# Kernel tuning notes

Measured on AMD Instinct MI355X. Metric: run time of the kernel, lower is better.

## Reference

```python
import jax, jax.numpy as jnp
import numpy as np

N = 100000      # nodes
E = 1600000     # edges (no self-loops by construction)
DIN, DH, DOUT = 128, 128, 64
EPS = 1e-8      # torch cosine_similarity eps
LN_EPS = 1e-5


def _segsum(v, idx, n=N):
    return jax.ops.segment_sum(v, idx, num_segments=n)


def att_coef(feats, row, col):
    """Edge-wise cosine-sim attention + degree norm + self-loop append (torch no_grad block).
    Returns fixed-shape (row2, col2, vals2) of length E+N; filtered edges get weight 0
    (equivalent to removal for all scatter_add / message-passing math)."""
    dot = jnp.einsum('ed,ed->e', feats[row], feats[col])            # [E]
    nrm = jnp.maximum(jnp.linalg.norm(feats, axis=1), EPS)          # [N]
    sims = dot / (nrm[row] * nrm[col])
    keep = sims >= 0.1                                              # row!=col guaranteed
    sims = jnp.where(keep, sims, 0.0)
    deg = _segsum(sims, row)
    dinv = jnp.where(deg > 0, deg ** -0.5, 0.0)                     # inf -> 0
    sims = dinv[row] * sims * dinv[col]
    deg_new = _segsum(keep.astype(feats.dtype), col) + 1.0          # [N], >= 1
    self_val = 1.0 / deg_new
    vals = jnp.where(keep, jnp.exp(sims), 0.0)                      # removed edges -> 0
    sl = jnp.arange(N)
    row2 = jnp.concatenate([row, sl])
    col2 = jnp.concatenate([col, sl])
    vals2 = jnp.concatenate([vals, jnp.exp(self_val)])
    return row2, col2, vals2


def gcn_conv(x, row, col, w, W, b):
    """PyG GCNConv (normalize=True, add_self_loops=False) with given edge_weight."""
    h = x @ W                                                        # [N, out]
    deg = _segsum(w, col)
    dinv = jnp.where(deg > 0, deg ** -0.5, 0.0)
    norm = dinv[row] * w * dinv[col]                                 # [E+N]
    out = _segsum(norm[:, None] * h[row], col)                       # scatter to targets
    return out + b


def layer_norm(x, g, b):
    mu = jnp.mean(x, axis=-1, keepdims=True)
    var = jnp.mean((x - mu) ** 2, axis=-1, keepdims=True)
    return (x - mu) * jax.lax.rsqrt(var + LN_EPS) * g + b


def setup_inputs() -> dict:
    key = jax.random.key(0)
    ks = jax.random.split(key, 6)
    x = jax.random.normal(ks[0], (N, DIN), jnp.float32)
    row = jax.random.randint(ks[1], (E,), 0, N)
    col = jax.random.randint(ks[2], (E,), 0, N)
    col = jnp.where(col == row, (col + 1) % N, col)                  # no self-loops
    s1 = float(np.sqrt(6.0 / (DIN + DH)))                            # glorot
    s2 = float(np.sqrt(6.0 / (DH + DOUT)))
    W1 = jax.random.uniform(ks[3], (DIN, DH), jnp.float32, -s1, s1)
    W2 = jax.random.uniform(ks[4], (DH, DOUT), jnp.float32, -s2, s2)
    return dict(x=x, row=row, col=col,
                W1=W1, b1=jnp.zeros((DH,), jnp.float32),
                ln_g=jnp.ones((DH,), jnp.float32), ln_b=jnp.zeros((DH,), jnp.float32),
                W2=W2, b2=jnp.zeros((DOUT,), jnp.float32))


def reference(x, row, col, W1, b1, ln_g, ln_b, W2, b2):
    # layer 1: att_coef (no_grad) -> GCNConv -> LayerNorm -> ReLU (dropout is eval no-op)
    r2, c2, v2 = att_coef(jax.lax.stop_gradient(x), row, col)
    h = gcn_conv(x, r2, c2, v2, W1, b1)
    h = jax.nn.relu(layer_norm(h, ln_g, ln_b))
    # layer 2: att_coef on updated features (original edge list), final conv + log_softmax
    r2, c2, v2 = att_coef(jax.lax.stop_gradient(h), row, col)
    out = gcn_conv(h, r2, c2, v2, W2, b2)
    return jax.nn.log_softmax(out, axis=-1)
```

## Files before the change

### kernel.cpp

```cpp
#include <hip/hip_runtime.h>
#include <math.h>

#define EPSF 1e-8f
#define LN_EPS 1e-5f
#define BL_MARGIN 0.002f

typedef unsigned int  u32;
typedef unsigned short u16;
typedef _Float16 h2_t __attribute__((ext_vector_type(2)));
typedef _Float16 half8_t __attribute__((ext_vector_type(8)));
typedef float f32x4_t __attribute__((ext_vector_type(4)));

static __device__ inline u32 pack_h2(float a, float b) {
    h2_t h; h.x = (_Float16)a; h.y = (_Float16)b;
    return __builtin_bit_cast(u32, h);
}
static __device__ inline float h2lo(u32 u) {
    return (float)__builtin_bit_cast(h2_t, u).x;
}
static __device__ inline float h2hi(u32 u) {
    return (float)__builtin_bit_cast(h2_t, u).y;
}

static __device__ inline f32x4_t mfma16(uint4 a, uint4 b, f32x4_t c) {
    return __builtin_amdgcn_mfma_f32_16x16x32_f16(
        __builtin_bit_cast(half8_t, a), __builtin_bit_cast(half8_t, b), c, 0, 0, 0);
}

__global__ __launch_bounds__(256) void cast_norm_k(const float* __restrict__ feat,
    u32* __restrict__ fhf, float* __restrict__ nrm, int n) {
    int wid  = (blockIdx.x * 256 + threadIdx.x) >> 6;
    int lane = threadIdx.x & 63;
    if (wid >= n) return;
    float2 v = *(const float2*)(feat + (size_t)wid * 128 + lane * 2);
    float s = v.x * v.x + v.y * v.y;
    #pragma unroll
    for (int off = 32; off; off >>= 1) s += __shfl_xor(s, off, 64);
    float nv = fmaxf(sqrtf(s), EPSF);
    float inv = 1.0f / nv;
    fhf[(size_t)wid * 64 + lane] = pack_h2(v.x * inv, v.y * inv);
    if (lane == 0) nrm[wid] = nv;
}


__global__ __launch_bounds__(256) void count_k(const int* __restrict__ col,
                                               int* __restrict__ cntAll, int ecnt) {
    int e = blockIdx.x * 256 + threadIdx.x;
    if (e < ecnt) atomicAdd(&cntAll[col[e]], 1);
}

__global__ __launch_bounds__(256) void scan1_k(const int* __restrict__ cnt,
    int* __restrict__ colStart, int* __restrict__ bsum, int n) {
    __shared__ int tmp[256];
    int i = blockIdx.x * 256 + threadIdx.x;
    int v = (i < n) ? cnt[i] : 0;
    tmp[threadIdx.x] = v; __syncthreads();
    for (int off = 1; off < 256; off <<= 1) {
        int t = (threadIdx.x >= off) ? tmp[threadIdx.x - off] : 0;
        __syncthreads();
        tmp[threadIdx.x] += t;
        __syncthreads();
    }
    if (i < n) colStart[i] = tmp[threadIdx.x] - v;
    if (threadIdx.x == 255) bsum[blockIdx.x] = tmp[255];
}

__global__ __launch_bounds__(512) void scan2_k(int* __restrict__ bsum, int nb) {
    __shared__ int tmp[512];
    int v = (threadIdx.x < nb) ? bsum[threadIdx.x] : 0;
    tmp[threadIdx.x] = v; __syncthreads();
    for (int off = 1; off < 512; off <<= 1) {
        int t = (threadIdx.x >= off) ? tmp[threadIdx.x - off] : 0;
        __syncthreads();
        tmp[threadIdx.x] += t;
        __syncthreads();
    }
    if (threadIdx.x < nb) bsum[threadIdx.x] = tmp[threadIdx.x] - v;
}

__global__ __launch_bounds__(256) void scan3_k(int* __restrict__ colStart,
    const int* __restrict__ bsum, int n) {
    int i = blockIdx.x * 256 + threadIdx.x;
    if (i < n) colStart[i] += bsum[blockIdx.x];
}

__global__ __launch_bounds__(256) void fill_k(const int* __restrict__ row,
    const int* __restrict__ col, const int* __restrict__ startAll,
    int* __restrict__ cur, int* __restrict__ rowAll, int ecnt) {
    int e = blockIdx.x * 256 + threadIdx.x;
    if (e >= ecnt) return;
    int c = col[e];
    int p = startAll[c] + atomicAdd(&cur[c], 1);
    rowAll[p] = row[e];
}

__global__ __launch_bounds__(256) void edge_dot_mf_k(const u32* __restrict__ fhf,
    const float* __restrict__ feat32,
    const int* __restrict__ rowAll, const int* __restrict__ startAll,
    const int* __restrict__ cntAll, const float* __restrict__ nrm,
    float* __restrict__ sims, float* __restrict__ deg1, int n) {
    int wid  = (blockIdx.x * 256 + threadIdx.x) >> 6;
    int lane = threadIdx.x & 63;
    if (wid >= n) return;
    int s0 = startAll[wid], cnt = cntAll[wid];
    if (cnt == 0) return;
    int lr = lane & 15;
    int kq = lane >> 4;
    const u32* fcp = fhf + (size_t)wid * 64 + kq * 4;
    uint4 a0 = *(const uint4*)(fcp);
    uint4 a1 = *(const uint4*)(fcp + 16);
    uint4 a2 = *(const uint4*)(fcp + 32);
    uint4 a3 = *(const uint4*)(fcp + 48);
    float nc = nrm[wid];
    int cm1 = cnt - 1;
    for (int jj = 0; jj < cnt; jj += 32) {
        int e1 = jj + lr;
        int r1 = rowAll[s0 + min(e1, cm1)];
        const u32* fr1 = fhf + (size_t)r1 * 64 + kq * 4;
        uint4 b0 = *(const uint4*)(fr1);
        uint4 b1 = *(const uint4*)(fr1 + 16);
        uint4 b2 = *(const uint4*)(fr1 + 32);
        uint4 b3 = *(const uint4*)(fr1 + 48);
        bool g2 = (jj + 16) < cnt;
        int e2 = jj + 16 + lr;
        int r2 = 0;
        uint4 c0, c1, c2, c3;
        if (g2) {
            r2 = rowAll[s0 + min(e2, cm1)];
            const u32* fr2 = fhf + (size_t)r2 * 64 + kq * 4;
            c0 = *(const uint4*)(fr2);
            c1 = *(const uint4*)(fr2 + 16);
            c2 = *(const uint4*)(fr2 + 32);
            c3 = *(const uint4*)(fr2 + 48);
        }
        f32x4_t acc = {0.f, 0.f, 0.f, 0.f};
        acc = mfma16(a0, b0, acc);
        acc = mfma16(a1, b1, acc);
        acc = mfma16(a2, b2, acc);
        acc = mfma16(a3, b3, acc);
        float p1 = acc[0];
        bool act1 = (kq == 0) && (e1 < cnt);
        float p2 = 0.0f;
        bool act2 = false;
        if (g2) {
            f32x4_t acc2 = {0.f, 0.f, 0.f, 0.f};
            acc2 = mfma16(a0, c0, acc2);
            acc2 = mfma16(a1, c1, acc2);
            acc2 = mfma16(a2, c2, acc2);
            acc2 = mfma16(a3, c3, acc2);
            p2 = acc2[0];
            act2 = (kq == 0) && (e2 < cnt);
        }
        unsigned long long bl = __ballot(act1 && fabsf(p1 - 0.1f) < BL_MARGIN);
        while (bl) {
            int src = __ffsll((unsigned long long)bl) - 1; bl &= bl - 1ull;
            int rt = __shfl(r1, src, 64);
            float2 xa = *(const float2*)(feat32 + (size_t)rt * 128 + lane * 2);
            float2 xb = *(const float2*)(feat32 + (size_t)wid * 128 + lane * 2);
            float s2 = xa.x * xb.x + xa.y * xb.y;
            #pragma unroll
            for (int off = 32; off; off >>= 1) s2 += __shfl_xor(s2, off, 64);
            float pf = s2 / (nrm[rt] * nc);
            if (lane == src) p1 = pf;
        }
        unsigned long long bl2 = __ballot(act2 && fabsf(p2 - 0.1f) < BL_MARGIN);
        while (bl2) {
            int src = __ffsll((unsigned long long)bl2) - 1; bl2 &= bl2 - 1ull;
            int rt = __shfl(r2, src, 64);
            float2 xa = *(const float2*)(feat32 + (size_t)rt * 128 + lane * 2);
            float2 xb = *(const float2*)(feat32 + (size_t)wid * 128 + lane * 2);
            float s2 = xa.x * xb.x + xa.y * xb.y;
            #pragma unroll
            for (int off = 32; off; off >>= 1) s2 += __shfl_xor(s2, off, 64);
            float pf = s2 / (nrm[rt] * nc);
            if (lane == src) p2 = pf;
        }
        if (act1) {
            float kv = (p1 >= 0.1f) ? p1 : 0.0f;
            sims[s0 + e1] = kv;
            if (kv > 0.0f) atomicAdd(&deg1[r1], kv);
        }
        if (act2) {
            float kv = (p2 >= 0.1f) ? p2 : 0.0f;
            sims[s0 + e2] = kv;
            if (kv > 0.0f) atomicAdd(&deg1[r2], kv);
        }
    }
}

__global__ __launch_bounds__(256) void edge_c_csr_k(const float* __restrict__ sims,
    const int* __restrict__ rowAll, const int* __restrict__ startAll,
    const int* __restrict__ cntAll, const float* __restrict__ deg1,
    int2* __restrict__ kv, int* __restrict__ cntK, float* __restrict__ dinv2,
    float* __restrict__ cself, int n) {
    int wid  = (blockIdx.x * 256 + threadIdx.x) >> 6;
    int lane = threadIdx.x & 63;
    if (wid >= n) return;
    int s0 = startAll[wid], cnt = cntAll[wid];
    float degc = deg1[wid];
    float d1c = (degc > 0.0f) ? 1.0f / sqrtf(degc) : 0.0f;
    float vsum = 0.0f; int kc = 0;
    for (int jj = 0; jj < cnt; jj += 64) {
        int j = jj + lane;
        bool keep = false; int r = 0; float v = 0.0f;
        if (j < cnt) {
            float s = sims[s0 + j];
            if (s > 0.0f) {
                r = rowAll[s0 + j];
                float dr = 1.0f / sqrtf(deg1[r]);
                v = expf(dr * s * d1c);
                keep = true;
            }
        }
        unsigned long long m = __ballot(keep ? 1 : 0);
        if (keep) {
            int pre = __popcll(m & ((1ull << lane) - 1ull));
            int2 pk; pk.x = r; pk.y = __float_as_int(v);
            kv[s0 + kc + pre] = pk;
            vsum += v;
        }
        kc += __popcll(m);
    }
    #pragma unroll
    for (int off = 32; off; off >>= 1) vsum += __shfl_xor(vsum, off, 64);
    if (lane == 0) {
        float ws_ = expf(1.0f / ((float)kc + 1.0f));
        float dg = ws_ + vsum;
        float di = 1.0f / sqrtf(dg);
        dinv2[wid] = di;
        cself[wid] = di * ws_;
        cntK[wid]  = kc;
    }
}


__global__ __launch_bounds__(256) void gemm128_k(const float* __restrict__ A,
    const float* __restrict__ W, const float* __restrict__ scale,
    float* __restrict__ out, int n) {
    __shared__ float Ws[128 * 64];
    int colBase = blockIdx.y * 64;
    for (int i = threadIdx.x; i < 128 * 64 / 4; i += 256) {
        int k = i >> 4, c4 = i & 15;
        ((float4*)Ws)[i] = *(const float4*)(W + k * 128 + colBase + c4 * 4);
    }
    __syncthreads();
    const int TPN = 16;
    int group = threadIdx.x / TPN;
    int tin   = threadIdx.x % TPN;
    int nid   = (blockIdx.x * 16 + group) * 4;
    if (nid >= n) return;
    int dbase = tin * 4;
    int nm1 = n - 1;
    const float4* a0 = (const float4*)(A + (size_t)min(nid,     nm1) * 128);
    const float4* a1 = (const float4*)(A + (size_t)min(nid + 1, nm1) * 128);
    const float4* a2 = (const float4*)(A + (size_t)min(nid + 2, nm1) * 128);
    const float4* a3 = (const float4*)(A + (size_t)min(nid + 3, nm1) * 128);
    float4 acc0 = {0,0,0,0}, acc1 = {0,0,0,0}, acc2 = {0,0,0,0}, acc3 = {0,0,0,0};
    #pragma unroll 2
    for (int k4 = 0; k4 < 32; ++k4) {
        const float* wr = Ws + (k4 * 4) * 64 + dbase;
        float4 w0 = *(const float4*)(wr);
        float4 w1 = *(const float4*)(wr + 64);
        float4 w2 = *(const float4*)(wr + 128);
        float4 w3 = *(const float4*)(wr + 192);
        float4 v0 = a0[k4], v1 = a1[k4], v2 = a2[k4], v3 = a3[k4];
        acc0.x += v0.x*w0.x + v0.y*w1.x + v0.z*w2.x + v0.w*w3.x;
        acc0.y += v0.x*w0.y + v0.y*w1.y + v0.z*w2.y + v0.w*w3.y;
        acc0.z += v0.x*w0.z + v0.y*w1.z + v0.z*w2.z + v0.w*w3.z;
        acc0.w += v0.x*w0.w + v0.y*w1.w + v0.z*w2.w + v0.w*w3.w;
        acc1.x += v1.x*w0.x + v1.y*w1.x + v1.z*w2.x + v1.w*w3.x;
        acc1.y += v1.x*w0.y + v1.y*w1.y + v1.z*w2.y + v1.w*w3.y;
        acc1.z += v1.x*w0.z + v1.y*w1.z + v1.z*w2.z + v1.w*w3.z;
        acc1.w += v1.x*w0.w + v1.y*w1.w + v1.z*w2.w + v1.w*w3.w;
        acc2.x += v2.x*w0.x + v2.y*w1.x + v2.z*w2.x + v2.w*w3.x;
        acc2.y += v2.x*w0.y + v2.y*w1.y + v2.z*w2.y + v2.w*w3.y;
        acc2.z += v2.x*w0.z + v2.y*w1.z + v2.z*w2.z + v2.w*w3.z;
        acc2.w += v2.x*w0.w + v2.y*w1.w + v2.z*w2.w + v2.w*w3.w;
        acc3.x += v3.x*w0.x + v3.y*w1.x + v3.z*w2.x + v3.w*w3.x;
        acc3.y += v3.x*w0.y + v3.y*w1.y + v3.z*w2.y + v3.w*w3.y;
        acc3.z += v3.x*w0.z + v3.y*w1.z + v3.z*w2.z + v3.w*w3.z;
        acc3.w += v3.x*w0.w + v3.y*w1.w + v3.z*w2.w + v3.w*w3.w;
    }
    float4 accs[4] = {acc0, acc1, acc2, acc3};
    #pragma unroll
    for (int i = 0; i < 4; ++i) {
        if (nid + i < n) {
            float sc = scale[nid + i];
            float4 r; r.x = accs[i].x * sc; r.y = accs[i].y * sc;
            r.z = accs[i].z * sc; r.w = accs[i].w * sc;
            *(float4*)(out + (size_t)(nid + i) * 128 + colBase + dbase) = r;
        }
    }
}

__global__ __launch_bounds__(256) void gemm64_hf_k(const float* __restrict__ A,
    const float* __restrict__ W, const float* __restrict__ scale,
    u32* __restrict__ outhf, int n) {
    __shared__ float Ws[128 * 32];
    int colBase = blockIdx.y * 32;
    for (int i = threadIdx.x; i < 128 * 32 / 4; i += 256) {
        int k = i >> 3, c4 = i & 7;
        ((float4*)Ws)[i] = *(const float4*)(W + k * 64 + colBase + c4 * 4);
    }
    __syncthreads();
    const int TPN = 8;
    int group = threadIdx.x / TPN;
    int tin   = threadIdx.x % TPN;
    int nid   = (blockIdx.x * 32 + group) * 4;
    if (nid >= n) return;
    int dbase = tin * 4;
    int nm1 = n - 1;
    const float4* a0 = (const float4*)(A + (size_t)min(nid,     nm1) * 128);
    const float4* a1 = (const float4*)(A + (size_t)min(nid + 1, nm1) * 128);
    const float4* a2 = (const float4*)(A + (size_t)min(nid + 2, nm1) * 128);
    const float4* a3 = (const float4*)(A + (size_t)min(nid + 3, nm1) * 128);
    float4 acc0 = {0,0,0,0}, acc1 = {0,0,0,0}, acc2 = {0,0,0,0}, acc3 = {0,0,0,0};
    #pragma unroll 2
    for (int k4 = 0; k4 < 32; ++k4) {
        const float* wr = Ws + (k4 * 4) * 32 + dbase;
        float4 w0 = *(const float4*)(wr);
        float4 w1 = *(const float4*)(wr + 32);
        float4 w2 = *(const float4*)(wr + 64);
        float4 w3 = *(const float4*)(wr + 96);
        float4 v0 = a0[k4], v1 = a1[k4], v2 = a2[k4], v3 = a3[k4];
        acc0.x += v0.x*w0.x + v0.y*w1.x + v0.z*w2.x + v0.w*w3.x;
        acc0.y += v0.x*w0.y + v0.y*w1.y + v0.z*w2.y + v0.w*w3.y;
        acc0.z += v0.x*w0.z + v0.y*w1.z + v0.z*w2.z + v0.w*w3.z;
        acc0.w += v0.x*w0.w + v0.y*w1.w + v0.z*w2.w + v0.w*w3.w;
        acc1.x += v1.x*w0.x + v1.y*w1.x + v1.z*w2.x + v1.w*w3.x;
        acc1.y += v1.x*w0.y + v1.y*w1.y + v1.z*w2.y + v1.w*w3.y;
        acc1.z += v1.x*w0.z + v1.y*w1.z + v1.z*w2.z + v1.w*w3.z;
        acc1.w += v1.x*w0.w + v1.y*w1.w + v1.z*w2.w + v1.w*w3.w;
        acc2.x += v2.x*w0.x + v2.y*w1.x + v2.z*w2.x + v2.w*w3.x;
        acc2.y += v2.x*w0.y + v2.y*w1.y + v2.z*w2.y + v2.w*w3.y;
        acc2.z += v2.x*w0.z + v2.y*w1.z + v2.z*w2.z + v2.w*w3.z;
        acc2.w += v2.x*w0.w + v2.y*w1.w + v2.z*w2.w + v2.w*w3.w;
        acc3.x += v3.x*w0.x + v3.y*w1.x + v3.z*w2.x + v3.w*w3.x;
        acc3.y += v3.x*w0.y + v3.y*w1.y + v3.z*w2.y + v3.w*w3.y;
        acc3.z += v3.x*w0.z + v3.y*w1.z + v3.z*w2.z + v3.w*w3.z;
        acc3.w += v3.x*w0.w + v3.y*w1.w + v3.z*w2.w + v3.w*w3.w;
    }
    float4 accs[4] = {acc0, acc1, acc2, acc3};
    #pragma unroll
    for (int i = 0; i < 4; ++i) {
        if (nid + i < n) {
            float sc = scale[nid + i];
            u32 o0 = pack_h2(accs[i].x * sc, accs[i].y * sc);
            u32 o1 = pack_h2(accs[i].z * sc, accs[i].w * sc);
            *(uint2*)(outhf + (size_t)(nid + i) * 32 + (colBase >> 1) + tin * 2)
                = make_uint2(o0, o1);
        }
    }
}


__global__ __launch_bounds__(256) void gather_ln_k(const float* __restrict__ hs,
    const int2* __restrict__ kv, const int* __restrict__ startAll,
    const int* __restrict__ cntK, const float* __restrict__ dinv2,
    const float* __restrict__ cself, const float* __restrict__ bias,
    const float* __restrict__ g, const float* __restrict__ bln,
    float* __restrict__ outbuf, u32* __restrict__ outhf,
    float* __restrict__ nrm, int n) {
    int wid = (blockIdx.x * 256 + threadIdx.x) >> 5;
    int l   = threadIdx.x & 31;
    if (wid >= n) return;
    int s0 = startAll[wid], k = cntK[wid];
    float4 acc = {0,0,0,0};
    int j = 0;
    for (; j + 7 < k; j += 8) {
        int2 p0 = kv[s0+j],   p1 = kv[s0+j+1], p2 = kv[s0+j+2], p3 = kv[s0+j+3];
        int2 p4 = kv[s0+j+4], p5 = kv[s0+j+5], p6 = kv[s0+j+6], p7 = kv[s0+j+7];
        float4 h0 = *(const float4*)(hs + (size_t)p0.x * 128 + l * 4);
        float4 h1 = *(const float4*)(hs + (size_t)p1.x * 128 + l * 4);
        float4 h2v = *(const float4*)(hs + (size_t)p2.x * 128 + l * 4);
        float4 h3 = *(const float4*)(hs + (size_t)p3.x * 128 + l * 4);
        float4 h4 = *(const float4*)(hs + (size_t)p4.x * 128 + l * 4);
        float4 h5 = *(const float4*)(hs + (size_t)p5.x * 128 + l * 4);
        float4 h6 = *(const float4*)(hs + (size_t)p6.x * 128 + l * 4);
        float4 h7 = *(const float4*)(hs + (size_t)p7.x * 128 + l * 4);
        float v0 = __int_as_float(p0.y), v1 = __int_as_float(p1.y);
        float v2 = __int_as_float(p2.y), v3 = __int_as_float(p3.y);
        float v4 = __int_as_float(p4.y), v5 = __int_as_float(p5.y);
        float v6 = __int_as_float(p6.y), v7 = __int_as_float(p7.y);
        acc.x += v0*h0.x + v1*h1.x + v2*h2v.x + v3*h3.x
               + v4*h4.x + v5*h5.x + v6*h6.x + v7*h7.x;
        acc.y += v0*h0.y + v1*h1.y + v2*h2v.y + v3*h3.y
               + v4*h4.y + v5*h5.y + v6*h6.y + v7*h7.y;
        acc.z += v0*h0.z + v1*h1.z + v2*h2v.z + v3*h3.z
               + v4*h4.z + v5*h5.z + v6*h6.z + v7*h7.z;
        acc.w += v0*h0.w + v1*h1.w + v2*h2v.w + v3*h3.w
               + v4*h4.w + v5*h5.w + v6*h6.w + v7*h7.w;
    }
    for (; j < k; ++j) {
        int2 p0 = kv[s0 + j];
        float4 h0 = *(const float4*)(hs + (size_t)p0.x * 128 + l * 4);
        float v0 = __int_as_float(p0.y);
        acc.x += v0*h0.x; acc.y += v0*h0.y; acc.z += v0*h0.z; acc.w += v0*h0.w;
    }
    float di = dinv2[wid], cs = cself[wid];
    float4 hsv = *(const float4*)(hs + (size_t)wid * 128 + l * 4);
    float4 vb  = *(const float4*)(bias + l * 4);
    float x0 = di*acc.x + cs*hsv.x + vb.x;
    float x1 = di*acc.y + cs*hsv.y + vb.y;
    float x2 = di*acc.z + cs*hsv.z + vb.z;
    float x3 = di*acc.w + cs*hsv.w + vb.w;
    float s = x0 + x1 + x2 + x3;
    #pragma unroll
    for (int off = 16; off; off >>= 1) s += __shfl_xor(s, off, 64);
    float mu = s * (1.0f / 128.0f);
    float d0 = x0 - mu, d1 = x1 - mu, d2 = x2 - mu, d3 = x3 - mu;
    float vv = d0*d0 + d1*d1 + d2*d2 + d3*d3;
    #pragma unroll
    for (int off = 16; off; off >>= 1) vv += __shfl_xor(vv, off, 64);
    float rstd = 1.0f / sqrtf(vv * (1.0f / 128.0f) + LN_EPS);
    float4 vg  = *(const float4*)(g + l * 4);
    float4 vbl = *(const float4*)(bln + l * 4);
    float y0 = fmaxf(d0 * rstd * vg.x + vbl.x, 0.0f);
    float y1 = fmaxf(d1 * rstd * vg.y + vbl.y, 0.0f);
    float y2 = fmaxf(d2 * rstd * vg.z + vbl.z, 0.0f);
    float y3 = fmaxf(d3 * rstd * vg.w + vbl.w, 0.0f);
    float4 yo; yo.x = y0; yo.y = y1; yo.z = y2; yo.w = y3;
    *(float4*)(outbuf + (size_t)wid * 128 + l * 4) = yo;
    float ns = y0*y0 + y1*y1 + y2*y2 + y3*y3;
    #pragma unroll
    for (int off = 16; off; off >>= 1) ns += __shfl_xor(ns, off, 64);
    float nv = fmaxf(sqrtf(ns), EPSF);
    float inv = 1.0f / nv;
    uint2 oh; oh.x = pack_h2(y0 * inv, y1 * inv); oh.y = pack_h2(y2 * inv, y3 * inv);
    *(uint2*)(outhf + (size_t)wid * 64 + l * 2) = oh;
    if (l == 0) nrm[wid] = nv;
}

__global__ __launch_bounds__(256) void gather_lsm_hf_k(const u32* __restrict__ g2s,
    const int2* __restrict__ kv, const int* __restrict__ startAll,
    const int* __restrict__ cntK, const float* __restrict__ dinv2,
    const float* __restrict__ cself, const float* __restrict__ b2,
    float* __restrict__ out, int n) {
    int wid = (blockIdx.x * 256 + threadIdx.x) >> 5;
    int l   = threadIdx.x & 31;
    if (wid >= n) return;
    int s0 = startAll[wid], k = cntK[wid];
    float acc0 = 0.f, acc1 = 0.f;
    int j = 0;
    for (; j + 7 < k; j += 8) {
        int2 p0 = kv[s0+j],   p1 = kv[s0+j+1], p2 = kv[s0+j+2], p3 = kv[s0+j+3];
        int2 p4 = kv[s0+j+4], p5 = kv[s0+j+5], p6 = kv[s0+j+6], p7 = kv[s0+j+7];
        u32 g0 = g2s[(size_t)p0.x * 32 + l];
        u32 g1 = g2s[(size_t)p1.x * 32 + l];
        u32 g2 = g2s[(size_t)p2.x * 32 + l];
        u32 g3 = g2s[(size_t)p3.x * 32 + l];
        u32 g4 = g2s[(size_t)p4.x * 32 + l];
        u32 g5 = g2s[(size_t)p5.x * 32 + l];
        u32 g6 = g2s[(size_t)p6.x * 32 + l];
        u32 g7 = g2s[(size_t)p7.x * 32 + l];
        float v0 = __int_as_float(p0.y), v1 = __int_as_float(p1.y);
        float v2 = __int_as_float(p2.y), v3 = __int_as_float(p3.y);
        float v4 = __int_as_float(p4.y), v5 = __int_as_float(p5.y);
        float v6 = __int_as_float(p6.y), v7 = __int_as_float(p7.y);
        acc0 += v0*h2lo(g0) + v1*h2lo(g1) + v2*h2lo(g2) + v3*h2lo(g3)
              + v4*h2lo(g4) + v5*h2lo(g5) + v6*h2lo(g6) + v7*h2lo(g7);
        acc1 += v0*h2hi(g0) + v1*h2hi(g1) + v2*h2hi(g2) + v3*h2hi(g3)
              + v4*h2hi(g4) + v5*h2hi(g5) + v6*h2hi(g6) + v7*h2hi(g7);
    }
    for (; j < k; ++j) {
        int2 p0 = kv[s0 + j];
        u32 g0 = g2s[(size_t)p0.x * 32 + l];
        float v0 = __int_as_float(p0.y);
        acc0 += v0 * h2lo(g0); acc1 += v0 * h2hi(g0);
    }
    float di = dinv2[wid], cs = cself[wid];
    u32 gsu = g2s[(size_t)wid * 32 + l];
    float2 vb = *(const float2*)(b2 + l * 2);
    float v0 = di * acc0 + cs * h2lo(gsu) + vb.x;
    float v1 = di * acc1 + cs * h2hi(gsu) + vb.y;
    float m = fmaxf(v0, v1);
    #pragma unroll
    for (int off = 16; off; off >>= 1) m = fmaxf(m, __shfl_xor(m, off, 64));
    float e = expf(v0 - m) + expf(v1 - m);
    #pragma unroll
    for (int off = 16; off; off >>= 1) e += __shfl_xor(e, off, 64);
    float lse = m + logf(e);
    *(float2*)(out + (size_t)wid * 64 + l * 2) = make_float2(v0 - lse, v1 - lse);
}


extern "C" void kernel_launch(void* const* d_in, const int* in_sizes, int n_in,
                              void* d_out, int out_size, void* d_ws, size_t ws_size,
                              hipStream_t stream) {
    (void)n_in; (void)out_size; (void)ws_size;
    const float* x   = (const float*)d_in[0];
    const int*   row = (const int*)d_in[1];
    const int*   col = (const int*)d_in[2];
    const float* W1  = (const float*)d_in[3];
    const float* b1  = (const float*)d_in[4];
    const float* lng = (const float*)d_in[5];
    const float* lnb = (const float*)d_in[6];
    const float* W2  = (const float*)d_in[7];
    const float* b2  = (const float*)d_in[8];
    float* out = (float*)d_out;

    const int N = in_sizes[0] / 128;
    const int E = in_sizes[1];

    int*   cntAll   = (int*)d_ws;
    int*   startAll = cntAll + N;
    int*   bsum     = startAll + N;
    float* nrm      = (float*)(bsum + 512);
    float* deg1     = nrm + N;
    float* dinv2    = deg1 + N;
    float* cself    = dinv2 + N;
    int*   cntK     = (int*)(cself + N);
    int*   rowAll   = cntK + N;
    int2*  kvp      = (int2*)(rowAll + E);
    u32*   fhf      = (u32*)(kvp + E);
    u32*   g2shf    = fhf + (size_t)64 * N;
    float* big      = (float*)(g2shf + (size_t)32 * N);
    float* sims     = big;
    float* hs       = big;
    float* h2       = big + (size_t)128 * N;

    const int nodeBlocks  = (N + 255) / 256;
    const int waveBlocks  = (N + 3) / 4;
    const int halfBlocks  = (N + 7) / 8;
    const int edgeBlocks  = (E + 255) / 256;
    const int scanBlocks  = nodeBlocks;

    hipMemsetAsync(cntAll, 0, (size_t)N * sizeof(int), stream);
    count_k<<<edgeBlocks, 256, 0, stream>>>(col, cntAll, E);
    scan1_k<<<scanBlocks, 256, 0, stream>>>(cntAll, startAll, bsum, N);
    scan2_k<<<1, 512, 0, stream>>>(bsum, scanBlocks);
    scan3_k<<<scanBlocks, 256, 0, stream>>>(startAll, bsum, N);
    hipMemsetAsync(cntK, 0, (size_t)N * sizeof(int), stream);
    fill_k<<<edgeBlocks, 256, 0, stream>>>(row, col, startAll, cntK, rowAll, E);

    hipMemsetAsync(deg1, 0, (size_t)N * sizeof(float), stream);
    cast_norm_k<<<waveBlocks, 256, 0, stream>>>(x, fhf, nrm, N);
    edge_dot_mf_k<<<waveBlocks, 256, 0, stream>>>(fhf, x, rowAll, startAll, cntAll, nrm,
                                                  sims, deg1, N);
    edge_c_csr_k<<<waveBlocks, 256, 0, stream>>>(sims, rowAll, startAll, cntAll, deg1,
                                                 kvp, cntK, dinv2, cself, N);
    gemm128_k<<<dim3((N + 63) / 64, 2), 256, 0, stream>>>(x, W1, dinv2, hs, N);
    gather_ln_k<<<halfBlocks, 256, 0, stream>>>(hs, kvp, startAll, cntK, dinv2, cself,
                                                b1, lng, lnb, h2, fhf, nrm, N);

    hipMemsetAsync(deg1, 0, (size_t)N * sizeof(float), stream);
    edge_dot_mf_k<<<waveBlocks, 256, 0, stream>>>(fhf, h2, rowAll, startAll, cntAll, nrm,
                                                  sims, deg1, N);
    edge_c_csr_k<<<waveBlocks, 256, 0, stream>>>(sims, rowAll, startAll, cntAll, deg1,
                                                 kvp, cntK, dinv2, cself, N);
    gemm64_hf_k<<<dim3((N + 127) / 128, 2), 256, 0, stream>>>(h2, W2, dinv2, g2shf, N);
    gather_lsm_hf_k<<<halfBlocks, 256, 0, stream>>>(g2shf, kvp, startAll, cntK, dinv2,
                                                    cself, b2, out, N);
}
```

Before: 720.0 us.

## Build CSR via two-level bucket sort instead of global atomic counting sort

```diff
diff --git a/kernel.cpp b/kernel.cpp
--- a/kernel.cpp
+++ b/kernel.cpp
@@ -4,6 +4,10 @@
 #define EPSF 1e-8f
 #define LN_EPS 1e-5f
 #define BL_MARGIN 0.002f
+
+#define BKT_SH 9
+#define CHUNK 4096
+#define DCAP 16384
 
 typedef unsigned int  u32;
 typedef unsigned short u16;
@@ -43,55 +47,136 @@
 }
 
 
-__global__ __launch_bounds__(256) void count_k(const int* __restrict__ col,
-                                               int* __restrict__ cntAll, int ecnt) {
-    int e = blockIdx.x * 256 + threadIdx.x;
-    if (e < ecnt) atomicAdd(&cntAll[col[e]], 1);
-}
-
-__global__ __launch_bounds__(256) void scan1_k(const int* __restrict__ cnt,
-    int* __restrict__ colStart, int* __restrict__ bsum, int n) {
+__global__ __launch_bounds__(256) void hist_k(const int* __restrict__ col,
+                                              int* __restrict__ bcnt, int ecnt) {
+    __shared__ int lc[256];
+    lc[threadIdx.x] = 0; __syncthreads();
+    for (int e = blockIdx.x * 256 + threadIdx.x; e < ecnt; e += gridDim.x * 256)
+        atomicAdd(&lc[col[e] >> BKT_SH], 1);
+    __syncthreads();
+    int v = lc[threadIdx.x];
+    if (v) atomicAdd(&bcnt[threadIdx.x], v);
+}
+
+__global__ __launch_bounds__(256) void bscan_k(const int* __restrict__ bcnt,
+    int* __restrict__ bstart, int* __restrict__ bcur) {
     __shared__ int tmp[256];
-    int i = blockIdx.x * 256 + threadIdx.x;
-    int v = (i < n) ? cnt[i] : 0;
-    tmp[threadIdx.x] = v; __syncthreads();
+    int t = threadIdx.x;
+    int v = bcnt[t];
+    tmp[t] = v; __syncthreads();
     for (int off = 1; off < 256; off <<= 1) {
-        int t = (threadIdx.x >= off) ? tmp[threadIdx.x - off] : 0;
+        int a = (t >= off) ? tmp[t - off] : 0;
         __syncthreads();
-        tmp[threadIdx.x] += t;
+        tmp[t] += a;
         __syncthreads();
     }
-    if (i < n) colStart[i] = tmp[threadIdx.x] - v;
-    if (threadIdx.x == 255) bsum[blockIdx.x] = tmp[255];
-}
-
-__global__ __launch_bounds__(512) void scan2_k(int* __restrict__ bsum, int nb) {
-    __shared__ int tmp[512];
-    int v = (threadIdx.x < nb) ? bsum[threadIdx.x] : 0;
-    tmp[threadIdx.x] = v; __syncthreads();
-    for (int off = 1; off < 512; off <<= 1) {
-        int t = (threadIdx.x >= off) ? tmp[threadIdx.x - off] : 0;
+    int ex = tmp[t] - v;
+    bstart[t] = ex; bcur[t] = ex;
+    if (t == 255) bstart[256] = tmp[255];
+}
+
+__global__ __launch_bounds__(256) void binfill_k(const int* __restrict__ row,
+    const int* __restrict__ col, int* __restrict__ bcur,
+    int2* __restrict__ ebuf, int ecnt) {
+    __shared__ int lc[256], ls[256], cur[256], gbase[256];
+    __shared__ int2 pairs[CHUNK];
+    __shared__ int dstv[CHUNK];
+    int t = threadIdx.x;
+    int e0 = blockIdx.x * CHUNK;
+    int m = min(CHUNK, ecnt - e0);
+    lc[t] = 0; cur[t] = 0; __syncthreads();
+    int myc[CHUNK / 256], myr[CHUNK / 256];
+    #pragma unroll
+    for (int i = 0; i < CHUNK / 256; ++i) {
+        int idx = t + i * 256;
+        if (idx < m) {
+            myc[i] = col[e0 + idx];
+            myr[i] = row[e0 + idx];
+            atomicAdd(&lc[myc[i] >> BKT_SH], 1);
+        }
+    }
+    __syncthreads();
+    int v = lc[t];
+    ls[t] = v; __syncthreads();
+    for (int off = 1; off < 256; off <<= 1) {
+        int a = (t >= off) ? ls[t - off] : 0;
         __syncthreads();
-        tmp[threadIdx.x] += t;
+        ls[t] += a;
         __syncthreads();
     }
-    if (threadIdx.x < nb) bsum[threadIdx.x] = tmp[threadIdx.x] - v;
-}
-
-__global__ __launch_bounds__(256) void scan3_k(int* __restrict__ colStart,
-    const int* __restrict__ bsum, int n) {
-    int i = blockIdx.x * 256 + threadIdx.x;
-    if (i < n) colStart[i] += bsum[blockIdx.x];
-}
-
-__global__ __launch_bounds__(256) void fill_k(const int* __restrict__ row,
-    const int* __restrict__ col, const int* __restrict__ startAll,
-    int* __restrict__ cur, int* __restrict__ rowAll, int ecnt) {
-    int e = blockIdx.x * 256 + threadIdx.x;
-    if (e >= ecnt) return;
-    int c = col[e];
-    int p = startAll[c] + atomicAdd(&cur[c], 1);
-    rowAll[p] = row[e];
+    int ex = ls[t] - v;
+    __syncthreads();
+    ls[t] = ex;
+    if (v) gbase[t] = atomicAdd(&bcur[t], v);
+    __syncthreads();
+    #pragma unroll
+    for (int i = 0; i < CHUNK / 256; ++i) {
+        int idx = t + i * 256;
+        if (idx < m) {
+            int b = myc[i] >> BKT_SH;
+            int s = ls[b] + atomicAdd(&cur[b], 1);
+            pairs[s] = make_int2(myc[i], myr[i]);
+            dstv[s]  = gbase[b] + (s - ls[b]);
+        }
+    }
+    __syncthreads();
+    for (int s = t; s < m; s += 256)
+        ebuf[dstv[s]] = pairs[s];
+}
+
+__global__ __launch_bounds__(256) void bucket_csr_k(const int2* __restrict__ ebuf,
+    const int* __restrict__ bstart, int* __restrict__ startAll,
+    int* __restrict__ cntAll, int* __restrict__ rowAll, int n) {
+    __shared__ int cnt[512], lst[512], cur[512];
+    __shared__ int rowbuf[DCAP];
+    int b = blockIdx.x, t = threadIdx.x;
+    int c0 = b << BKT_SH;
+    int s0 = bstart[b], s1 = bstart[b + 1];
+    int m = s1 - s0;
+    cnt[t] = 0; cnt[t + 256] = 0; cur[t] = 0; cur[t + 256] = 0;
+    __syncthreads();
+    for (int i = t; i < m; i += 256)
+        atomicAdd(&cnt[ebuf[s0 + i].x - c0], 1);
+    __syncthreads();
+    int v0 = cnt[t], v1 = cnt[t + 256];
+    lst[t] = v0; lst[t + 256] = v1; __syncthreads();
+    for (int off = 1; off < 256; off <<= 1) {
+        int a0 = (t >= off) ? lst[t - off] : 0;
+        int a1 = (t >= off) ? lst[256 + t - off] : 0;
+        __syncthreads();
+        lst[t] += a0; lst[t + 256] += a1;
+        __syncthreads();
+    }
+    int h0 = lst[255];
+    int e0x = lst[t] - v0;
+    int e1x = lst[t + 256] - v1 + h0;
+    __syncthreads();
+    lst[t] = e0x; lst[t + 256] = e1x;
+    __syncthreads();
+    #pragma unroll
+    for (int half = 0; half < 2; ++half) {
+        int i = t + half * 256;
+        int c = c0 + i;
+        if (c < n) { startAll[c] = s0 + lst[i]; cntAll[c] = cnt[i]; }
+    }
+    if (m <= DCAP) {
+        for (int i = t; i < m; i += 256) {
+            int2 p = ebuf[s0 + i];
+            int ci = p.x - c0;
+            int pos = lst[ci] + atomicAdd(&cur[ci], 1);
+            rowbuf[pos] = p.y;
+        }
+        __syncthreads();
+        for (int i = t; i < m; i += 256)
+            rowAll[s0 + i] = rowbuf[i];
+    } else {
+        for (int i = t; i < m; i += 256) {
+            int2 p = ebuf[s0 + i];
+            int ci = p.x - c0;
+            int pos = lst[ci] + atomicAdd(&cur[ci], 1);
+            rowAll[s0 + pos] = p.y;
+        }
+    }
 }
 
 __global__ __launch_bounds__(256) void edge_dot_mf_k(const u32* __restrict__ fhf,
@@ -504,8 +589,10 @@
 
     int*   cntAll   = (int*)d_ws;
     int*   startAll = cntAll + N;
-    int*   bsum     = startAll + N;
-    float* nrm      = (float*)(bsum + 512);
+    int*   bcnt     = startAll + N;
+    int*   bstart   = bcnt + 256;
+    int*   bcur     = bstart + 257;
+    float* nrm      = (float*)(bcnt + 1024);
     float* deg1     = nrm + N;
     float* dinv2    = deg1 + N;
     float* cself    = dinv2 + N;
@@ -518,20 +605,17 @@
     float* sims     = big;
     float* hs       = big;
     float* h2       = big + (size_t)128 * N;
-
-    const int nodeBlocks  = (N + 255) / 256;
+    int2*  ebuf     = kvp;
+
     const int waveBlocks  = (N + 3) / 4;
     const int halfBlocks  = (N + 7) / 8;
-    const int edgeBlocks  = (E + 255) / 256;
-    const int scanBlocks  = nodeBlocks;
-
-    hipMemsetAsync(cntAll, 0, (size_t)N * sizeof(int), stream);
-    count_k<<<edgeBlocks, 256, 0, stream>>>(col, cntAll, E);
-    scan1_k<<<scanBlocks, 256, 0, stream>>>(cntAll, startAll, bsum, N);
-    scan2_k<<<1, 512, 0, stream>>>(bsum, scanBlocks);
-    scan3_k<<<scanBlocks, 256, 0, stream>>>(startAll, bsum, N);
-    hipMemsetAsync(cntK, 0, (size_t)N * sizeof(int), stream);
-    fill_k<<<edgeBlocks, 256, 0, stream>>>(row, col, startAll, cntK, rowAll, E);
+    const int NB          = (N + 511) >> 9;
+
+    hipMemsetAsync(bcnt, 0, 256 * sizeof(int), stream);
+    hist_k<<<256, 256, 0, stream>>>(col, bcnt, E);
+    bscan_k<<<1, 256, 0, stream>>>(bcnt, bstart, bcur);
+    binfill_k<<<(E + CHUNK - 1) / CHUNK, 256, 0, stream>>>(row, col, bcur, ebuf, E);
+    bucket_csr_k<<<NB, 256, 0, stream>>>(ebuf, bstart, startAll, cntAll, rowAll, N);
 
     hipMemsetAsync(deg1, 0, (size_t)N * sizeof(float), stream);
     cast_norm_k<<<waveBlocks, 256, 0, stream>>>(x, fhf, nrm, N);
```

After: 616.6 us. -14.4%, faster.
